# Optimization experiments

Hardware: AMD Instinct MI355X
Metric: run time of the kernel (lower is better)

## Reference

```python
import jax, jax.numpy as jnp
import numpy as np

N = 20000          # num proposals (nodes)
E = 320000         # num edges
IN = 4096          # roi feature dim
EMB = 200          # glove embed dim
HID = 512          # hidden dim
NH = 8             # heads (conv1)
HC = HID // NH     # 64 per-head channels
NCLS = 151         # VG object classes
NEG_SLOPE = 0.2    # PyG GATConv leaky_relu slope


def setup_inputs() -> dict:
    key = jax.random.key(0)
    ks = jax.random.split(key, 18)
    d_in1 = IN + EMB + 128  # 4424, conv1 input dim
    inp = {
        "roi_features": jax.random.normal(ks[0], (N, IN), jnp.float32),
        "box_info": jax.random.uniform(ks[1], (N, 9), jnp.float32),
        # embedding tables
        "emb1": jax.random.normal(ks[2], (NCLS, EMB), jnp.float32) * 0.02,
        "emb2": jax.random.normal(ks[3], (NCLS, EMB), jnp.float32) * 0.02,
        # bbox MLP 9 -> 32 -> 128
        "bw1": jax.random.normal(ks[4], (9, 32), jnp.float32) / np.sqrt(9),
        "bb1": jnp.zeros((32,), jnp.float32),
        "bw2": jax.random.normal(ks[5], (32, 128), jnp.float32) / np.sqrt(32),
        "bb2": jnp.zeros((128,), jnp.float32),
        # GATConv1: d_in1 -> 8 heads x 64, concat
        "W1": jax.random.normal(ks[6], (d_in1, NH * HC), jnp.float32) / np.sqrt(d_in1),
        "a_src1": jax.random.normal(ks[7], (NH, HC), jnp.float32) * 0.1,
        "a_dst1": jax.random.normal(ks[8], (NH, HC), jnp.float32) * 0.1,
        "bias1": jnp.zeros((NH * HC,), jnp.float32),
        # GATConv2: 512 -> 512, 1 head, concat=False
        "W2": jax.random.normal(ks[9], (HID, HID), jnp.float32) / np.sqrt(HID),
        "a_src2": jax.random.normal(ks[10], (1, HID), jnp.float32) * 0.1,
        "a_dst2": jax.random.normal(ks[11], (1, HID), jnp.float32) * 0.1,
        "bias2": jnp.zeros((HID,), jnp.float32),
        # int inputs
        "obj_labels": jax.random.randint(ks[12], (N,), 0, NCLS, jnp.int32),
        "edge_index": jax.random.randint(ks[13], (2, E), 0, N, jnp.int32),
    }
    return inp


def _segment_softmax(logits, seg, n):
    # logits: [E, H]; softmax over edges sharing the same destination seg id
    m = jax.ops.segment_max(logits, seg, num_segments=n)
    e = jnp.exp(logits - m[seg])
    s = jax.ops.segment_sum(e, seg, num_segments=n)
    return e / (s[seg] + 1e-16)


def _gat_conv(x, src, dst, W, a_src, a_dst, bias, concat):
    # PyG GATConv (self-loops already included in src/dst); dropout off (eval)
    n = x.shape[0]
    H, C = a_src.shape
    h = (x @ W).reshape(n, H, C)                      # [N, H, C]
    al_s = jnp.einsum('nhc,hc->nh', h, a_src)         # [N, H]
    al_d = jnp.einsum('nhc,hc->nh', h, a_dst)
    logits = jax.nn.leaky_relu(al_s[src] + al_d[dst], NEG_SLOPE)  # [E, H]
    alpha = _segment_softmax(logits, dst, n)          # [E, H]
    out = jax.ops.segment_sum(alpha[:, :, None] * h[src], dst, num_segments=n)
    out = out.reshape(n, H * C) if concat else out.mean(axis=1)
    return out + bias


def reference(roi_features, box_info, emb1, emb2, bw1, bb1, bw2, bb2,
              W1, a_src1, a_dst1, bias1, W2, a_src2, a_dst2, bias2,
              obj_labels, edge_index):
    n = roi_features.shape[0]
    # predcls mode: GT labels -> embedding lookup
    obj_embed = emb1[obj_labels]                              # [N, 200]
    pos = jax.nn.relu(box_info @ bw1 + bb1)
    pos = jax.nn.relu(pos @ bw2 + bb2)                        # [N, 128]
    x = jnp.concatenate([roi_features, obj_embed, pos], -1)  # [N, 4424]

    # add self-loops (PyG GATConv default)
    ar = jnp.arange(n, dtype=edge_index.dtype)
    src = jnp.concatenate([edge_index[0], ar])
    dst = jnp.concatenate([edge_index[1], ar])

    edge_f1 = jax.nn.elu(_gat_conv(x, src, dst, W1, a_src1, a_dst1, bias1, True))
    obj_feats = _gat_conv(edge_f1, src, dst, W2, a_src2, a_dst2, bias2, False)

    obj_dists = jax.nn.one_hot(obj_labels, NCLS, dtype=jnp.float32)
    edge_pre_rep = jnp.concatenate([roi_features, obj_feats, emb2[obj_labels]], -1)
    return obj_dists, obj_labels, edge_pre_rep
```

## Files before the change

kernel.cpp:

```cpp
#include <hip/hip_runtime.h>
#include <hip/hip_bf16.h>

#define NNODES 20000
#define NEDGES 320000
#define ETOT   (NEDGES + NNODES)
#define KPADX  4224
#define MPAD   20096
#define NCLS   151
#define EPRW   4808
#define OUT_LAB_OFF  3020000L
#define OUT_EPR_OFF  3040000L
#define NSLOPE 0.2f

typedef __attribute__((ext_vector_type(8))) short bf16x8;
typedef __attribute__((ext_vector_type(4))) float f32x4;
typedef __attribute__((ext_vector_type(4))) short s16x4;

__device__ __forceinline__ short f2bf(float v) {
  union { __hip_bfloat16 b; short s; } u;
  u.b = __float2bfloat16(v);
  return u.s;
}

__device__ __forceinline__ float bf2f(short s) {
  union { float f; unsigned u; } x;
  x.u = ((unsigned)(unsigned short)s) << 16;
  return x.f;
}

__device__ __forceinline__ void gld16(const short* g, short* l) {
  __builtin_amdgcn_global_load_lds(
      (const __attribute__((address_space(1))) unsigned int*)g,
      (__attribute__((address_space(3))) unsigned int*)l, 16, 0, 0);
}

#define PB0 20000
#define PB1 (PB0 + 1584)
#define PB2 (PB1 + 2112)
#define PB3 (PB2 + 256)
#define PB4 (PB3 + 1329)
#define PB5 (PB4 + 151)

__global__ __launch_bounds__(256) void mega_prep_kernel(
    const float* __restrict__ roi, const float* __restrict__ box,
    const float* __restrict__ emb1, const float* __restrict__ emb2,
    const float* __restrict__ bw1, const float* __restrict__ bb1,
    const float* __restrict__ bw2, const float* __restrict__ bb2,
    const float* __restrict__ W1, const float* __restrict__ W2,
    const int* __restrict__ labels, const int* __restrict__ ei,
    short* __restrict__ x, short* __restrict__ w1t, short* __restrict__ w2t,
    short* __restrict__ ef1, int* __restrict__ deg,
    float* __restrict__ als1, float* __restrict__ ald1,
    float* __restrict__ als2, float* __restrict__ ald2,
    float* __restrict__ E1, float* __restrict__ dout) {
  const int b = blockIdx.x;
  const int tid = threadIdx.x;

  __shared__ float hid[32];
  __shared__ float bx[9];
  __shared__ float tile[32][33];

  if (b < PB0) {
    const int n = b;
    if (tid < 9) bx[tid] = box[n * 9 + tid];
    __syncthreads();
    if (tid < 32) {
      float a = bb1[tid];
#pragma unroll
      for (int i = 0; i < 9; ++i) a += bx[i] * bw1[i * 32 + tid];
      hid[tid] = a > 0.f ? a : 0.f;
    }
    __syncthreads();
    const long xrow = (long)n * KPADX;
    if (tid < 128) {
      float a = bb2[tid];
#pragma unroll
      for (int i = 0; i < 32; ++i) a += hid[i] * bw2[i * 128 + tid];
      a = a > 0.f ? a : 0.f;
      x[xrow + 4096 + tid] = f2bf(a);
    }
    const int lab = labels[n];
    float* epr = dout + OUT_EPR_OFF + (long)n * EPRW;
#pragma unroll
    for (int j = tid * 4; j < 4096; j += 1024) {
      const f32x4 v = *(const f32x4*)&roi[(long)n * 4096 + j];
      __builtin_nontemporal_store(v, (f32x4*)&epr[j]);
      s16x4 bb;
      bb.x = f2bf(v.x); bb.y = f2bf(v.y); bb.z = f2bf(v.z); bb.w = f2bf(v.w);
      __builtin_nontemporal_store(bb, (s16x4*)&x[xrow + j]);
    }
    if (tid < 50) {
      const int j = tid * 4;
      const f32x4 e2 = *(const f32x4*)&emb2[lab * 200 + j];
      __builtin_nontemporal_store(e2, (f32x4*)&epr[4608 + j]);
    }
    for (int j = tid; j < NCLS; j += 256)
      dout[(long)n * NCLS + j] = (j == lab) ? 1.f : 0.f;
    if (tid == 0) dout[OUT_LAB_OFF + n] = (float)lab;
  } else if (b < PB1) {
    const int t = (b - PB0) * 256 + tid;
    if (t < 96 * KPADX) x[(long)NNODES * KPADX + t] = 0;
    if (t < 96 * 512)   ef1[(long)NNODES * 512 + t] = 0;
    if (t < MPAD * 8)   { als1[t] = 0.f; ald1[t] = 0.f; }
    if (t < MPAD)       { als2[t] = 0.f; ald2[t] = 0.f; }
  } else if (b < PB2) {
    const int t = b - PB1;
    const int n0 = (t % 16) * 32;
    const int k0 = (t / 16) * 32;
    const int tx = tid & 31, ty = tid >> 5;
#pragma unroll
    for (int i = ty; i < 32; i += 8) {
      const int kp = k0 + i;
      const int src = kp < 4096 ? kp : kp + 200;
      tile[i][tx] = W1[(long)src * 512 + (n0 + tx)];
    }
    __syncthreads();
#pragma unroll
    for (int i = ty; i < 32; i += 8)
      w1t[(long)(n0 + i) * KPADX + (k0 + tx)] = f2bf(tile[tx][i]);
  } else if (b < PB3) {
    const int t = b - PB2;
    const int n0 = (t % 16) * 32;
    const int k0 = (t / 16) * 32;
    const int tx = tid & 31, ty = tid >> 5;
#pragma unroll
    for (int i = ty; i < 32; i += 8)
      tile[i][tx] = W2[(long)(k0 + i) * 512 + (n0 + tx)];
    __syncthreads();
#pragma unroll
    for (int i = ty; i < 32; i += 8)
      w2t[(long)(n0 + i) * 512 + (k0 + tx)] = f2bf(tile[tx][i]);
  } else if (b < PB4) {
    const int e = (b - PB3) * 256 + tid;
    if (e < ETOT) {
      const int d = (e < NEDGES) ? ei[NEDGES + e] : (e - NEDGES);
      atomicAdd(&deg[d], 1);
    }
  } else {
    const int c = b - PB4;
#pragma unroll
    for (int jj = 0; jj < 2; ++jj) {
      const int j = tid + jj * 256;
      float a = 0.f;
      for (int k = 0; k < 200; ++k)
        a += emb1[c * 200 + k] * W1[(long)(4096 + k) * 512 + j];
      E1[c * 512 + j] = a;
    }
  }
}

__global__ __launch_bounds__(256) void scan_kernel(const int* __restrict__ deg,
                                                   int* __restrict__ off,
                                                   int* __restrict__ cur) {
  __shared__ int part[256];
  const int tid = threadIdx.x;
  const int chunk = (NNODES + 255) / 256;
  int start = tid * chunk;
  int end = start + chunk; if (end > NNODES) end = NNODES;
  int s = 0;
  for (int i = start; i < end; ++i) s += deg[i];
  part[tid] = s;
  __syncthreads();
  for (int d = 1; d < 256; d <<= 1) {
    const int v = (tid >= d) ? part[tid - d] : 0;
    __syncthreads();
    part[tid] += v;
    __syncthreads();
  }
  int base = part[tid] - s;
  for (int i = start; i < end; ++i) { off[i] = base; cur[i] = base; base += deg[i]; }
}

__global__ __launch_bounds__(256) void gemm_bt(const short* __restrict__ A,
                                               const short* __restrict__ BT,
                                               short* __restrict__ C,
                                               const float* __restrict__ aS,
                                               const float* __restrict__ aD,
                                               float* __restrict__ als,
                                               float* __restrict__ ald,
                                               const float* __restrict__ E1,
                                               const int* __restrict__ labels,
                                               const int* __restrict__ ei,
                                               int* __restrict__ cur,
                                               int* __restrict__ csrs,
                                               int Kpad, int Ncols, int H,
                                               int nbx) {
  const int tid = threadIdx.x;
  const int ngemm = nbx * (Ncols >> 7);
  if ((int)blockIdx.x >= ngemm) {
    if (ei) {
      const int e = ((int)blockIdx.x - ngemm) * 256 + tid;
      if (e < ETOT) {
        const int s = (e < NEDGES) ? ei[e] : (e - NEDGES);
        const int d = (e < NEDGES) ? ei[NEDGES + e] : (e - NEDGES);
        unsigned slot = (unsigned)atomicAdd(&cur[d], 1);
        if (slot >= ETOT) slot = 0;
        csrs[slot] = s;
      }
    }
    return;
  }
  __shared__ short As[4096];
  __shared__ short Bs[4096];
  const int lane = tid & 63;
  const int w = tid >> 6;
  const int wr = w >> 1, wc = w & 1;
  const long bm = (long)((int)blockIdx.x % nbx) * 128;
  const long bn = (long)((int)blockIdx.x / nbx) * 128;

  f32x4 acc[4][4] = {};

  const short* gA0 = A + (bm + w * 32 + (lane >> 2)) * (long)Kpad + (lane & 3) * 8;
  const short* gA1 = gA0 + 16L * Kpad;
  const short* gB0 = BT + (bn + w * 32 + (lane >> 2)) * (long)Kpad + (lane & 3) * 8;
  const short* gB1 = gB0 + 16L * Kpad;
  short* lA0 = &As[w * 1024];
  short* lA1 = &As[w * 1024 + 512];
  short* lB0 = &Bs[w * 1024];
  short* lB1 = &Bs[w * 1024 + 512];

  const int ar = (wr * 64 + (lane & 15)) * 32 + (lane >> 4) * 8;
  const int br = (wc * 64 + (lane & 15)) * 32 + (lane >> 4) * 8;

  for (int k0 = 0; k0 < Kpad; k0 += 32) {
    gld16(gA0, lA0); gld16(gA1, lA1);
    gld16(gB0, lB0); gld16(gB1, lB1);
    gA0 += 32; gA1 += 32; gB0 += 32; gB1 += 32;
    asm volatile("s_waitcnt vmcnt(0)" ::: "memory");
    __syncthreads();
    bf16x8 a[4], b[4];
#pragma unroll
    for (int mi = 0; mi < 4; ++mi) a[mi] = *(const bf16x8*)&As[ar + mi * 512];
#pragma unroll
    for (int ni = 0; ni < 4; ++ni) b[ni] = *(const bf16x8*)&Bs[br + ni * 512];
#pragma unroll
    for (int mi = 0; mi < 4; ++mi)
#pragma unroll
      for (int ni = 0; ni < 4; ++ni)
        acc[mi][ni] = __builtin_amdgcn_mfma_f32_16x16x32_bf16(a[mi], b[ni], acc[mi][ni], 0, 0, 0);
    __syncthreads();
  }

  const int colb = (int)bn + wc * 64 + (lane & 15);

  if (E1) {
#pragma unroll
    for (int mi = 0; mi < 4; ++mi) {
#pragma unroll
      for (int r = 0; r < 4; ++r) {
        const long row = bm + wr * 64 + mi * 16 + (lane >> 4) * 4 + r;
        const int lb = (row < NNODES) ? labels[row] : 0;
        const float* e1r = E1 + (long)lb * 512;
#pragma unroll
        for (int ni = 0; ni < 4; ++ni)
          acc[mi][ni][r] += e1r[colb + ni * 16];
      }
    }
  }

#pragma unroll
  for (int mi = 0; mi < 4; ++mi) {
#pragma unroll
    for (int ni = 0; ni < 4; ++ni) {
      const long row0 = bm + wr * 64 + mi * 16 + (lane >> 4) * 4;
      const long col  = bn + wc * 64 + ni * 16 + (lane & 15);
#pragma unroll
      for (int r = 0; r < 4; ++r)
        C[(row0 + r) * (long)Ncols + col] = f2bf(acc[mi][ni][r]);
    }
  }

  float asv[4], adv[4];
#pragma unroll
  for (int ni = 0; ni < 4; ++ni) {
    asv[ni] = aS[colb + ni * 16];
    adv[ni] = aD[colb + ni * 16];
  }
  const int head = (H == 8) ? (((int)bn >> 6) + wc) : 0;
#pragma unroll
  for (int mi = 0; mi < 4; ++mi) {
#pragma unroll
    for (int r = 0; r < 4; ++r) {
      float s = 0.f, d = 0.f;
#pragma unroll
      for (int ni = 0; ni < 4; ++ni) {
        const float v = acc[mi][ni][r];
        s += v * asv[ni];
        d += v * adv[ni];
      }
#pragma unroll
      for (int o = 1; o < 16; o <<= 1) {
        s += __shfl_xor(s, o);
        d += __shfl_xor(d, o);
      }
      if ((lane & 15) == 0) {
        const long row = bm + wr * 64 + mi * 16 + (lane >> 4) * 4 + r;
        atomicAdd(&als[row * H + head], s);
        atomicAdd(&ald[row * H + head], d);
      }
    }
  }
}

__global__ __launch_bounds__(256) void gather1_kernel(const int* __restrict__ off,
    const int* __restrict__ csrs,
    const float* __restrict__ als, const float* __restrict__ ald,
    const short* __restrict__ h1, const float* __restrict__ bias,
    short* __restrict__ ef1) {
  const int dn = blockIdx.x * 4 + (threadIdx.x >> 6);
  const int lane = threadIdx.x & 63;
  const int c0 = lane * 8;
  const int head = lane >> 3;
  const int beg = off[dn];
  const int end = (dn == NNODES - 1) ? ETOT : off[dn + 1];
  const float ad = ald[dn * 8 + head];
  float sum = 0.f;
  float acc[8] = {};
  for (int i = beg; i < end; ++i) {
    int s = csrs[i];
    if ((unsigned)s >= NNODES) s = 0;
    float l = als[s * 8 + head] + ad;
    l = l > 0.f ? l : NSLOPE * l;
    const float wgt = expf(l);
    sum += wgt;
    const bf16x8 hv = *(const bf16x8*)&h1[(long)s * 512 + c0];
#pragma unroll
    for (int j = 0; j < 8; ++j) acc[j] += wgt * bf2f(hv[j]);
  }
  const float inv = 1.f / (sum + 1e-16f);
  bf16x8 outv;
#pragma unroll
  for (int j = 0; j < 8; ++j) {
    float r = acc[j] * inv + bias[c0 + j];
    r = r > 0.f ? r : expm1f(r);
    outv[j] = f2bf(r);
  }
  *(bf16x8*)&ef1[(long)dn * 512 + c0] = outv;
}

__global__ __launch_bounds__(256) void gather2_kernel(const int* __restrict__ off,
    const int* __restrict__ csrs,
    const float* __restrict__ als, const float* __restrict__ ald,
    const short* __restrict__ h2, const float* __restrict__ bias,
    float* __restrict__ dout) {
  const int dn = blockIdx.x * 4 + (threadIdx.x >> 6);
  const int lane = threadIdx.x & 63;
  const int c0 = lane * 8;
  const int beg = off[dn];
  const int end = (dn == NNODES - 1) ? ETOT : off[dn + 1];
  const float ad = ald[dn];
  float sum = 0.f;
  float acc[8] = {};
  for (int i = beg; i < end; ++i) {
    int s = csrs[i];
    if ((unsigned)s >= NNODES) s = 0;
    float l = als[s] + ad;
    l = l > 0.f ? l : NSLOPE * l;
    const float wgt = expf(l);
    sum += wgt;
    const bf16x8 hv = *(const bf16x8*)&h2[(long)s * 512 + c0];
#pragma unroll
    for (int j = 0; j < 8; ++j) acc[j] += wgt * bf2f(hv[j]);
  }
  const float inv = 1.f / (sum + 1e-16f);
  float* epr = dout + OUT_EPR_OFF + (long)dn * EPRW + 4096;
  f32x4 o0, o1;
  o0.x = acc[0] * inv + bias[c0 + 0];
  o0.y = acc[1] * inv + bias[c0 + 1];
  o0.z = acc[2] * inv + bias[c0 + 2];
  o0.w = acc[3] * inv + bias[c0 + 3];
  o1.x = acc[4] * inv + bias[c0 + 4];
  o1.y = acc[5] * inv + bias[c0 + 5];
  o1.z = acc[6] * inv + bias[c0 + 6];
  o1.w = acc[7] * inv + bias[c0 + 7];
  __builtin_nontemporal_store(o0, (f32x4*)&epr[c0]);
  __builtin_nontemporal_store(o1, (f32x4*)&epr[c0 + 4]);
}

extern "C" void kernel_launch(void* const* d_in, const int* in_sizes, int n_in,
                              void* d_out, int out_size, void* d_ws, size_t ws_size,
                              hipStream_t stream) {
  const float* roi  = (const float*)d_in[0];
  const float* box  = (const float*)d_in[1];
  const float* emb1 = (const float*)d_in[2];
  const float* emb2 = (const float*)d_in[3];
  const float* bw1  = (const float*)d_in[4];
  const float* bb1  = (const float*)d_in[5];
  const float* bw2  = (const float*)d_in[6];
  const float* bb2  = (const float*)d_in[7];
  const float* W1   = (const float*)d_in[8];
  const float* as1  = (const float*)d_in[9];
  const float* ad1  = (const float*)d_in[10];
  const float* b1   = (const float*)d_in[11];
  const float* W2   = (const float*)d_in[12];
  const float* as2  = (const float*)d_in[13];
  const float* ad2  = (const float*)d_in[14];
  const float* b2   = (const float*)d_in[15];
  const int* labels = (const int*)d_in[16];
  const int* ei     = (const int*)d_in[17];
  float* dout = (float*)d_out;

  char* wsb = (char*)d_ws;
  size_t o = 0;
  auto alloc = [&](size_t bytes) -> void* {
    void* p = wsb + o;
    o += (bytes + 255) & ~(size_t)255;
    return p;
  };
  short* x    = (short*)alloc((size_t)MPAD * KPADX * 2);
  short* w1t  = (short*)alloc((size_t)512 * KPADX * 2);
  short* h1   = (short*)alloc((size_t)MPAD * 512 * 2);
  short* ef1  = (short*)alloc((size_t)MPAD * 512 * 2);
  short* w2t  = (short*)alloc((size_t)512 * 512 * 2);
  short* h2   = (short*)alloc((size_t)MPAD * 512 * 2);
  float* als1 = (float*)alloc((size_t)MPAD * 8 * 4);
  float* ald1 = (float*)alloc((size_t)MPAD * 8 * 4);
  float* als2 = (float*)alloc((size_t)MPAD * 4);
  float* ald2 = (float*)alloc((size_t)MPAD * 4);
  float* E1   = (float*)alloc((size_t)NCLS * 512 * 4);
  int*   deg  = (int*)alloc((size_t)NNODES * 4);
  int*   offs = (int*)alloc((size_t)NNODES * 4);
  int*   cur  = (int*)alloc((size_t)NNODES * 4);
  int*   csrs = (int*)alloc((size_t)ETOT * 4);

  const int EB = (ETOT + 255) / 256;

  hipMemsetAsync(deg, 0, (size_t)NNODES * 4, stream);

  hipLaunchKernelGGL(mega_prep_kernel, dim3(PB5), dim3(256), 0, stream,
                     roi, box, emb1, emb2, bw1, bb1, bw2, bb2, W1, W2,
                     labels, ei, x, w1t, w2t, ef1, deg,
                     als1, ald1, als2, ald2, E1, dout);
  hipLaunchKernelGGL(scan_kernel, dim3(1), dim3(256), 0, stream, deg, offs, cur);
  hipLaunchKernelGGL(gemm_bt, dim3(157 * 4 + EB), dim3(256), 0, stream,
                     x, w1t, h1, as1, ad1, als1, ald1, E1, labels,
                     ei, cur, csrs, KPADX, 512, 8, 157);
  hipLaunchKernelGGL(gather1_kernel, dim3(NNODES / 4), dim3(256), 0, stream,
                     offs, csrs, als1, ald1, h1, b1, ef1);
  hipLaunchKernelGGL(gemm_bt, dim3(157 * 4), dim3(256), 0, stream,
                     ef1, w2t, h2, as2, ad2, als2, ald2,
                     (const float*)nullptr, (const int*)nullptr,
                     (const int*)nullptr, (int*)nullptr, (int*)nullptr,
                     512, 512, 1, 157);
  hipLaunchKernelGGL(gather2_kernel, dim3(NNODES / 4), dim3(256), 0, stream,
                     offs, csrs, als2, ald2, h2, b2, dout);
}
```

Measured before the change: 646.1 us.

## Split CSR fill out of GEMM, reorder GEMM block mapping, cache x stores

The CSR scatter blocks that were appended to the first GEMM launch now run as their own kernel before the GEMM. The GEMM block index mapping changes from M-major to N-major, so the four column blocks that share an A row tile run next to each other and can reuse it from cache. The bf16 x writes in the prep kernel switch from nontemporal to regular stores, so the freshly written activations can stay in cache for the GEMM that follows. These changes add one kernel launch and remove the overlap between the atomic scatter and the GEMM.

Measured after the change: 654.8 us. No clear change (+1.3%).

```diff
diff --git a/kernel.cpp b/kernel.cpp
--- a/kernel.cpp
+++ b/kernel.cpp
@@ -87,7 +87,7 @@
       __builtin_nontemporal_store(v, (f32x4*)&epr[j]);
       s16x4 bb;
       bb.x = f2bf(v.x); bb.y = f2bf(v.y); bb.z = f2bf(v.z); bb.w = f2bf(v.w);
-      __builtin_nontemporal_store(bb, (s16x4*)&x[xrow + j]);
+      *(s16x4*)&x[xrow + j] = bb;
     }
     if (tid < 50) {
       const int j = tid * 4;
@@ -171,6 +171,17 @@
   for (int i = start; i < end; ++i) { off[i] = base; cur[i] = base; base += deg[i]; }
 }
 
+__global__ void csr_fill_kernel(const int* __restrict__ ei, int* __restrict__ cur,
+                                int* __restrict__ csrs) {
+  const int e = blockIdx.x * 256 + threadIdx.x;
+  if (e >= ETOT) return;
+  const int s = (e < NEDGES) ? ei[e] : (e - NEDGES);
+  const int d = (e < NEDGES) ? ei[NEDGES + e] : (e - NEDGES);
+  unsigned slot = (unsigned)atomicAdd(&cur[d], 1);
+  if (slot >= ETOT) slot = 0;
+  csrs[slot] = s;
+}
+
 __global__ __launch_bounds__(256) void gemm_bt(const short* __restrict__ A,
                                                const short* __restrict__ BT,
                                                short* __restrict__ C,
@@ -180,33 +191,16 @@
                                                float* __restrict__ ald,
                                                const float* __restrict__ E1,
                                                const int* __restrict__ labels,
-                                               const int* __restrict__ ei,
-                                               int* __restrict__ cur,
-                                               int* __restrict__ csrs,
-                                               int Kpad, int Ncols, int H,
-                                               int nbx) {
-  const int tid = threadIdx.x;
-  const int ngemm = nbx * (Ncols >> 7);
-  if ((int)blockIdx.x >= ngemm) {
-    if (ei) {
-      const int e = ((int)blockIdx.x - ngemm) * 256 + tid;
-      if (e < ETOT) {
-        const int s = (e < NEDGES) ? ei[e] : (e - NEDGES);
-        const int d = (e < NEDGES) ? ei[NEDGES + e] : (e - NEDGES);
-        unsigned slot = (unsigned)atomicAdd(&cur[d], 1);
-        if (slot >= ETOT) slot = 0;
-        csrs[slot] = s;
-      }
-    }
-    return;
-  }
+                                               int Kpad, int Ncols, int H) {
   __shared__ short As[4096];
   __shared__ short Bs[4096];
+  const int tid = threadIdx.x;
   const int lane = tid & 63;
   const int w = tid >> 6;
   const int wr = w >> 1, wc = w & 1;
-  const long bm = (long)((int)blockIdx.x % nbx) * 128;
-  const long bn = (long)((int)blockIdx.x / nbx) * 128;
+  const int nbn = Ncols >> 7;
+  const long bm = (long)((int)blockIdx.x / nbn) * 128;
+  const long bn = (long)((int)blockIdx.x % nbn) * 128;
 
   f32x4 acc[4][4] = {};
 
@@ -432,16 +426,16 @@
                      labels, ei, x, w1t, w2t, ef1, deg,
                      als1, ald1, als2, ald2, E1, dout);
   hipLaunchKernelGGL(scan_kernel, dim3(1), dim3(256), 0, stream, deg, offs, cur);
-  hipLaunchKernelGGL(gemm_bt, dim3(157 * 4 + EB), dim3(256), 0, stream,
+  hipLaunchKernelGGL(csr_fill_kernel, dim3(EB), dim3(256), 0, stream, ei, cur, csrs);
+  hipLaunchKernelGGL(gemm_bt, dim3(157 * 4), dim3(256), 0, stream,
                      x, w1t, h1, as1, ad1, als1, ald1, E1, labels,
-                     ei, cur, csrs, KPADX, 512, 8, 157);
+                     KPADX, 512, 8);
   hipLaunchKernelGGL(gather1_kernel, dim3(NNODES / 4), dim3(256), 0, stream,
                      offs, csrs, als1, ald1, h1, b1, ef1);
   hipLaunchKernelGGL(gemm_bt, dim3(157 * 4), dim3(256), 0, stream,
                      ef1, w2t, h2, as2, ad2, als2, ald2,
                      (const float*)nullptr, (const int*)nullptr,
-                     (const int*)nullptr, (int*)nullptr, (int*)nullptr,
-                     512, 512, 1, 157);
+                     512, 512, 1);
   hipLaunchKernelGGL(gather2_kernel, dim3(NNODES / 4), dim3(256), 0, stream,
                      offs, csrs, als2, ald2, h2, b2, dout);
 }
```
